# Optimization experiments

Measured on AMD Instinct MI355X. Metric: run time of the kernel, lower is better.

The kernel has to match this reference:

```python
import jax, jax.numpy as jnp
import numpy as np

T, D, I, E, K = 2048, 2048, 5632, 8, 2


def setup_inputs() -> dict:
    key = jax.random.key(0)
    k1, k2, k3, k4, k5 = jax.random.split(key, 5)
    s = 0.02
    return {
        "x": jax.random.normal(k1, (T, D), dtype=jnp.float32),
        "gate_w": jax.random.normal(k2, (E, D), dtype=jnp.float32) * s,
        "w_gate": jax.random.normal(k3, (E, I, D), dtype=jnp.float32) * s,
        "w_up": jax.random.normal(k4, (E, I, D), dtype=jnp.float32) * s,
        "w_down": jax.random.normal(k5, (E, D, I), dtype=jnp.float32) * s,
    }


def reference(x, gate_w, w_gate, w_up, w_down):
    # Router: logits [T, E], top-k then softmax over the k selected logits
    logits = x @ gate_w.T
    top_vals, top_idx = jax.lax.top_k(logits, K)          # [T, K]
    rw = jax.nn.softmax(top_vals, axis=-1)                # [T, K]
    # Dense combine weights [T, E]: sum of routing weights over selected slots.
    # Mathematically identical to the per-(expert, slot) scatter-add in torch,
    # since duplicate selections of the same expert just sum their weights.
    combine = jnp.sum(jax.nn.one_hot(top_idx, E, dtype=x.dtype) * rw[..., None], axis=1)  # [T, E]
    # SwiGLU expert MLPs, batched over experts (grouped GEMM as dense einsum)
    g = jnp.einsum("td,eid->tei", x, w_gate)              # [T, E, I]
    u = jnp.einsum("td,eid->tei", x, w_up)                # [T, E, I]
    h = jax.nn.silu(g) * u                                 # [T, E, I]
    out_e = jnp.einsum("tei,edi->ted", h, w_down)         # [T, E, D]
    return jnp.einsum("ted,te->td", out_e, combine)       # [T, D]
```

## Files before the change

### kernel.cpp

```cpp
#include <hip/hip_runtime.h>
#include <hip/hip_bf16.h>
#include <stdint.h>

#define TTOK 2048
#define DDIM 2048
#define IDIM 5632
#define NEXP 8

typedef __attribute__((ext_vector_type(8))) short bf16x8;
typedef __attribute__((ext_vector_type(4))) float f32x4;
typedef __attribute__((ext_vector_type(8))) unsigned short u16x8;
typedef __attribute__((ext_vector_type(4))) unsigned short u16x4;

__device__ __forceinline__ unsigned short f2bf(float f) {
  union { float f; uint32_t u; } v; v.f = f;
  uint32_t u = v.u + 0x7fffu + ((v.u >> 16) & 1u);
  return (unsigned short)(u >> 16);
}

__device__ __forceinline__ uint32_t fbits(float f) {
  union { float f; uint32_t u; } v; v.f = f; return v.u;
}

__device__ __forceinline__ u16x8 cvt8t(float4 a, float4 b) {
  union { u16x8 v; uint32_t w[4]; } r;
  r.w[0] = __builtin_amdgcn_perm(fbits(a.y), fbits(a.x), 0x07060302);
  r.w[1] = __builtin_amdgcn_perm(fbits(a.w), fbits(a.z), 0x07060302);
  r.w[2] = __builtin_amdgcn_perm(fbits(b.y), fbits(b.x), 0x07060302);
  r.w[3] = __builtin_amdgcn_perm(fbits(b.w), fbits(b.z), 0x07060302);
  return r.v;
}

typedef __attribute__((address_space(3))) void lds_t;
typedef const __attribute__((address_space(1))) void gbl_t;
__device__ __forceinline__ void gload16(const void* g, void* l) {
  __builtin_amdgcn_global_load_lds((gbl_t*)g, (lds_t*)l, 16, 0, 0);
}

#define PIPE_WAIT_BAR() asm volatile("s_waitcnt vmcnt(8) lgkmcnt(0)\n\ts_barrier" ::: "memory")

__global__ __launch_bounds__(256) void router_kernel(
    const float* __restrict__ x, const float* __restrict__ gw,
    unsigned short* __restrict__ xbf,
    int* __restrict__ cnt, int* __restrict__ slots, float* __restrict__ wts)
{
  const int lane = threadIdx.x & 63;
  const int t = (blockIdx.x * blockDim.x + threadIdx.x) >> 6;
  const float* xr = x + (size_t)t * DDIM;
  float acc[NEXP];
#pragma unroll
  for (int e = 0; e < NEXP; ++e) acc[e] = 0.f;
#pragma unroll
  for (int it = 0; it < DDIM / 256; ++it) {
    const int d = (it * 64 + lane) * 4;
    const float4 xv = *(const float4*)(xr + d);
    u16x4 xb; xb[0]=f2bf(xv.x); xb[1]=f2bf(xv.y); xb[2]=f2bf(xv.z); xb[3]=f2bf(xv.w);
    *(u16x4*)(xbf + (size_t)t * DDIM + d) = xb;
#pragma unroll
    for (int e = 0; e < NEXP; ++e) {
      const float4 gv = *(const float4*)(gw + (size_t)e * DDIM + d);
      acc[e] += xv.x*gv.x + xv.y*gv.y + xv.z*gv.z + xv.w*gv.w;
    }
  }
#pragma unroll
  for (int e = 0; e < NEXP; ++e) {
    float v = acc[e];
#pragma unroll
    for (int off = 32; off > 0; off >>= 1) v += __shfl_xor(v, off);
    acc[e] = v;
  }
  if (lane == 0) {
    int i0 = 0; float v0 = acc[0];
#pragma unroll
    for (int e = 1; e < NEXP; ++e) if (acc[e] > v0) { v0 = acc[e]; i0 = e; }
    int i1 = -1; float v1 = -3.4e38f;
#pragma unroll
    for (int e = 0; e < NEXP; ++e) { if (e == i0) continue; if (acc[e] > v1) { v1 = acc[e]; i1 = e; } }
    const float e1 = __expf(v1 - v0);
    const float w0 = 1.f / (1.f + e1);
    const float w1 = e1 / (1.f + e1);
    const int p0 = atomicAdd(&cnt[i0], 1);
    slots[i0 * TTOK + p0] = t * 2;     wts[i0 * TTOK + p0] = w0;
    const int p1 = atomicAdd(&cnt[i1], 1);
    slots[i1 * TTOK + p1] = t * 2 + 1; wts[i1 * TTOK + p1] = w1;
  }
}

__global__ void plan_kernel(const int* __restrict__ cnt,
                            int* __restrict__ tilemap, int* __restrict__ ntiles)
{
  if (threadIdx.x == 0 && blockIdx.x == 0) {
    int n = 0;
#pragma unroll
    for (int e = 0; e < NEXP; ++e) {
      const int nt = (cnt[e] + 255) >> 8;
      for (int m = 0; m < nt; ++m) tilemap[n++] = (e << 8) | m;
    }
    ntiles[0] = n;
  }
}


__global__ __launch_bounds__(512, 2) void gateup_kernel(
    const unsigned short* __restrict__ xbf,
    const float* __restrict__ wg, const float* __restrict__ wu,
    const int* __restrict__ cnt, const int* __restrict__ slots,
    const int* __restrict__ tilemap, const int* __restrict__ ntiles,
    unsigned short* __restrict__ h)
{
  const int flat = (blockIdx.x & 7) * 132 + (blockIdx.x >> 3);
  const int ti = flat % 24;
  if (ti >= ntiles[0]) return;
  const int em = tilemap[ti];
  const int e = em >> 8;
  const int mt = em & 255;
  const int n0 = (flat / 24) * 128;
  const int count = cnt[e];
  const int m0 = mt * 256;

  __shared__ unsigned short A[2][256][64];
  __shared__ unsigned short Bg[2][128][64];
  __shared__ unsigned short Bu[2][128][64];
  __shared__ int rslot[256];
  __shared__ int rtok[256];

  const int tid = threadIdx.x;
  const int lane = tid & 63;
  const int wid = tid >> 6;

  if (tid < 256) {
    const int idx = m0 + tid;
    const int safe = slots[e * TTOK + m0];
    const int s = (idx < count) ? slots[e * TTOK + idx] : safe;
    rslot[tid] = (idx < count) ? s : -1;
    rtok[tid] = s >> 1;
  }
  __syncthreads();

  const int aswz = ((lane & 7) ^ ((lane >> 3) & 7)) * 8;
  const unsigned short* aptr[4];
#pragma unroll
  for (int j = 0; j < 4; ++j) {
    const int arow = j * 64 + wid * 8 + (lane >> 3);
    aptr[j] = xbf + (size_t)rtok[arow] * DDIM + aswz;
  }

  const int brow = tid >> 2;
  const int bcb = (tid & 3) * 2;
  const int bswz = brow & 7;
  const size_t wboff = (size_t)e * IDIM * DDIM + (size_t)(n0 + brow) * DDIM + bcb * 8;
  const float* gsrc = wg + wboff;
  const float* usrc = wu + wboff;

  const int wr = wid >> 2;
  const int wc = wid & 3;
  const int fr = lane & 15;
  const int kc = lane >> 4;
  const int rsw = fr & 7;

  f32x4 accg[8][2] = {};
  f32x4 accu[8][2] = {};

  float4 Pg[4], Pu[4];
#pragma unroll
  for (int j = 0; j < 4; ++j) gload16(aptr[j], &A[0][j * 64 + wid * 8][0]);
#pragma unroll
  for (int q = 0; q < 4; ++q) { Pg[q] = *(const float4*)(gsrc + q * 4); Pu[q] = *(const float4*)(usrc + q * 4); }
#pragma unroll
  for (int qq = 0; qq < 2; ++qq) {
    const int oc = ((bcb + qq) ^ bswz) * 8;
    *(u16x8*)&Bg[0][brow][oc] = cvt8t(Pg[qq * 2], Pg[qq * 2 + 1]);
    *(u16x8*)&Bu[0][brow][oc] = cvt8t(Pu[qq * 2], Pu[qq * 2 + 1]);
  }
#pragma unroll
  for (int q = 0; q < 4; ++q) { Pg[q] = *(const float4*)(gsrc + 64 + q * 4); Pu[q] = *(const float4*)(usrc + 64 + q * 4); }
  PIPE_WAIT_BAR();

#pragma unroll 2
  for (int t = 0; t < 32; ++t) {
    const int cur = t & 1;
    const int kp  = (t + 1 <= 31) ? (t + 1) * 64 : 31 * 64;
    const int kp2 = (t + 2 <= 31) ? (t + 2) * 64 : 31 * 64;

#pragma unroll
    for (int j = 0; j < 4; ++j) gload16(aptr[j] + kp, &A[cur ^ 1][j * 64 + wid * 8][0]);
    __builtin_amdgcn_sched_barrier(0);
#pragma unroll
    for (int qq = 0; qq < 2; ++qq) {
      const int oc = ((bcb + qq) ^ bswz) * 8;
      *(u16x8*)&Bg[cur ^ 1][brow][oc] = cvt8t(Pg[qq * 2], Pg[qq * 2 + 1]);
      *(u16x8*)&Bu[cur ^ 1][brow][oc] = cvt8t(Pu[qq * 2], Pu[qq * 2 + 1]);
    }
#pragma unroll
    for (int q = 0; q < 4; ++q) { Pg[q] = *(const float4*)(gsrc + kp2 + q * 4); Pu[q] = *(const float4*)(usrc + kp2 + q * 4); }
    __builtin_amdgcn_sched_barrier(0);

#pragma unroll
    for (int kk = 0; kk < 2; ++kk) {
      bf16x8 a[8], bg[2], bu[2];
      const int cs = ((kk * 4 + kc) ^ rsw) * 8;
#pragma unroll
      for (int mf = 0; mf < 8; ++mf)
        a[mf] = *(const bf16x8*)&A[cur][wr * 128 + mf * 16 + fr][cs];
#pragma unroll
      for (int nf = 0; nf < 2; ++nf) {
        bg[nf] = *(const bf16x8*)&Bg[cur][wc * 32 + nf * 16 + fr][cs];
        bu[nf] = *(const bf16x8*)&Bu[cur][wc * 32 + nf * 16 + fr][cs];
      }
      __builtin_amdgcn_s_setprio(1);
#pragma unroll
      for (int mf = 0; mf < 8; ++mf)
#pragma unroll
        for (int nf = 0; nf < 2; ++nf) {
          accg[mf][nf] = __builtin_amdgcn_mfma_f32_16x16x32_bf16(a[mf], bg[nf], accg[mf][nf], 0, 0, 0);
          accu[mf][nf] = __builtin_amdgcn_mfma_f32_16x16x32_bf16(a[mf], bu[nf], accu[mf][nf], 0, 0, 0);
        }
      __builtin_amdgcn_s_setprio(0);
    }

    PIPE_WAIT_BAR();
  }

#pragma unroll
  for (int mf = 0; mf < 8; ++mf)
#pragma unroll
    for (int nf = 0; nf < 2; ++nf)
#pragma unroll
      for (int j = 0; j < 4; ++j) {
        const int r = wr * 128 + mf * 16 + (lane >> 4) * 4 + j;
        const int s = rslot[r];
        if (s >= 0) {
          const float g = accg[mf][nf][j];
          const float u = accu[mf][nf][j];
          const float hv = g / (1.f + __expf(-g)) * u;
          h[(size_t)s * IDIM + n0 + wc * 32 + nf * 16 + fr] = f2bf(hv);
        }
      }
}

__global__ __launch_bounds__(512, 2) void down_kernel(
    const unsigned short* __restrict__ h,
    const float* __restrict__ wd,
    const int* __restrict__ cnt, const int* __restrict__ slots,
    const float* __restrict__ wts,
    const int* __restrict__ tilemap, const int* __restrict__ ntiles,
    float* __restrict__ out)
{
  const int flat = (blockIdx.x & 7) * 96 + (blockIdx.x >> 3);
  const int ti = flat % 24;
  if (ti >= ntiles[0]) return;
  const int em = tilemap[ti];
  const int e = em >> 8;
  const int mt = em & 255;
  const int rest = flat / 24;
  const int n0 = (rest & 7) * 256;
  const int kbase = (rest >> 3) * (IDIM / 4);
  const int count = cnt[e];
  const int m0 = mt * 256;

  __shared__ unsigned short A[2][256][64];
  __shared__ unsigned short B[2][256][64];
  __shared__ int rslot[256];
  __shared__ float rw[256];

  const int tid = threadIdx.x;
  const int lane = tid & 63;
  const int wid = tid >> 6;

  if (tid < 256) {
    const int idx = m0 + tid;
    const int safe = slots[e * TTOK + m0];
    const int s = (idx < count) ? slots[e * TTOK + idx] : safe;
    rslot[tid] = (idx < count) ? s : (safe | 0x40000000);
    rw[tid] = (idx < count) ? wts[e * TTOK + idx] : 0.f;
  }
  __syncthreads();

  const int aswz = ((lane & 7) ^ ((lane >> 3) & 7)) * 8;
  const unsigned short* aptr[4];
#pragma unroll
  for (int j = 0; j < 4; ++j) {
    const int arow = j * 64 + wid * 8 + (lane >> 3);
    aptr[j] = h + (size_t)(rslot[arow] & 0x3fffffff) * IDIM + kbase + aswz;
  }

  const int brow = tid >> 1;
  const int bcb = (tid & 1) * 4;
  const int bswz = brow & 7;
  const float* bsrc = wd + (size_t)e * DDIM * IDIM + (size_t)(n0 + brow) * IDIM + kbase + bcb * 8;

  const int wr = wid >> 2;
  const int wc = wid & 3;
  const int fr = lane & 15;
  const int kc = lane >> 4;
  const int rsw = fr & 7;

  f32x4 acc[8][4] = {};

  float4 Pb[8];
#pragma unroll
  for (int j = 0; j < 4; ++j) gload16(aptr[j], &A[0][j * 64 + wid * 8][0]);
#pragma unroll
  for (int q = 0; q < 8; ++q) Pb[q] = *(const float4*)(bsrc + q * 4);
#pragma unroll
  for (int qq = 0; qq < 4; ++qq)
    *(u16x8*)&B[0][brow][((bcb + qq) ^ bswz) * 8] = cvt8t(Pb[qq * 2], Pb[qq * 2 + 1]);
#pragma unroll
  for (int q = 0; q < 8; ++q) Pb[q] = *(const float4*)(bsrc + 64 + q * 4);
  PIPE_WAIT_BAR();

#pragma unroll 2
  for (int t = 0; t < 22; ++t) {
    const int cur = t & 1;
    const int kp  = (t + 1 <= 21) ? (t + 1) * 64 : 21 * 64;
    const int kp2 = (t + 2 <= 21) ? (t + 2) * 64 : 21 * 64;

#pragma unroll
    for (int j = 0; j < 4; ++j) gload16(aptr[j] + kp, &A[cur ^ 1][j * 64 + wid * 8][0]);
    __builtin_amdgcn_sched_barrier(0);
#pragma unroll
    for (int qq = 0; qq < 4; ++qq)
      *(u16x8*)&B[cur ^ 1][brow][((bcb + qq) ^ bswz) * 8] = cvt8t(Pb[qq * 2], Pb[qq * 2 + 1]);
#pragma unroll
    for (int q = 0; q < 8; ++q) Pb[q] = *(const float4*)(bsrc + kp2 + q * 4);
    __builtin_amdgcn_sched_barrier(0);

#pragma unroll
    for (int kk = 0; kk < 2; ++kk) {
      bf16x8 a[8], b[4];
      const int cs = ((kk * 4 + kc) ^ rsw) * 8;
#pragma unroll
      for (int mf = 0; mf < 8; ++mf)
        a[mf] = *(const bf16x8*)&A[cur][wr * 128 + mf * 16 + fr][cs];
#pragma unroll
      for (int nf = 0; nf < 4; ++nf)
        b[nf] = *(const bf16x8*)&B[cur][wc * 64 + nf * 16 + fr][cs];
      __builtin_amdgcn_s_setprio(1);
#pragma unroll
      for (int mf = 0; mf < 8; ++mf)
#pragma unroll
        for (int nf = 0; nf < 4; ++nf)
          acc[mf][nf] = __builtin_amdgcn_mfma_f32_16x16x32_bf16(a[mf], b[nf], acc[mf][nf], 0, 0, 0);
      __builtin_amdgcn_s_setprio(0);
    }

    PIPE_WAIT_BAR();
  }

#pragma unroll
  for (int mf = 0; mf < 8; ++mf)
#pragma unroll
    for (int j = 0; j < 4; ++j) {
      const int r = wr * 128 + mf * 16 + (lane >> 4) * 4 + j;
      const int s = rslot[r];
      if (!(s & 0x40000000)) {
        const int t2 = s >> 1;
        const float w = rw[r];
#pragma unroll
        for (int nf = 0; nf < 4; ++nf)
          atomicAdd(out + (size_t)t2 * DDIM + n0 + wc * 64 + nf * 16 + fr,
                    acc[mf][nf][j] * w);
      }
    }
}

extern "C" void kernel_launch(void* const* d_in, const int* in_sizes, int n_in,
                              void* d_out, int out_size, void* d_ws, size_t ws_size,
                              hipStream_t stream) {
  const float* x  = (const float*)d_in[0];
  const float* gw = (const float*)d_in[1];
  const float* wg = (const float*)d_in[2];
  const float* wu = (const float*)d_in[3];
  const float* wd = (const float*)d_in[4];
  float* out = (float*)d_out;

  char* ws = (char*)d_ws;
  unsigned short* xbf = (unsigned short*)ws;
  unsigned short* h   = (unsigned short*)(ws + 8388608);
  int*   slots = (int*)(ws + 8388608 + 46137344);
  float* wts   = (float*)(ws + 8388608 + 46137344 + 65536);
  int*   cnt   = (int*)(ws + 8388608 + 46137344 + 131072);
  int*   tmap  = (int*)(ws + 8388608 + 46137344 + 131072 + 32);
  int*   ntl   = (int*)(ws + 8388608 + 46137344 + 131072 + 288);

  hipMemsetAsync(cnt, 0, NEXP * sizeof(int), stream);
  hipMemsetAsync(d_out, 0, (size_t)TTOK * DDIM * sizeof(float), stream);

  router_kernel<<<TTOK / 4, 256, 0, stream>>>(x, gw, xbf, cnt, slots, wts);
  plan_kernel<<<1, 64, 0, stream>>>(cnt, tmap, ntl);
  gateup_kernel<<<1056, 512, 0, stream>>>(xbf, wg, wu, cnt, slots, tmap, ntl, h);
  down_kernel<<<768, 512, 0, stream>>>(h, wd, cnt, slots, wts, tmap, ntl, out);
}
```

Before: 816.9 us.

## Restructure MoE GEMM pipelines into phased MFMA/load interleave with contiguous h layout

Both grouped GEMM kernels now split each K step into four barrier-separated phases, each issuing part of the next tile's global loads and LDS writes and then a quarter of the MFMAs. This is meant to overlap memory traffic with matrix work more finely. Gate and up weights share one 256-row B tile with a single accumulator array, and the SiLU*up combine happens through an LDS exchange after the loop. The h intermediate is laid out contiguously per expert using prefix offsets from the plan kernel, so down_kernel reads A rows sequentially instead of gathering by slot. In exchange there are many more barriers per iteration and an extra LDS round trip in the epilogue.

```diff
diff --git a/kernel.cpp b/kernel.cpp
--- a/kernel.cpp
+++ b/kernel.cpp
@@ -37,7 +37,37 @@
   __builtin_amdgcn_global_load_lds((gbl_t*)g, (lds_t*)l, 16, 0, 0);
 }
 
-#define PIPE_WAIT_BAR() asm volatile("s_waitcnt vmcnt(8) lgkmcnt(0)\n\ts_barrier" ::: "memory")
+#define WRITE_B(buf, hh, r0, r1, r2, r3) do {                                  \
+    *(u16x8*)&SB[buf][(hh)*128 + brow][((bcb + 0) ^ bswz) * 8] = cvt8t(r0, r1);\
+    *(u16x8*)&SB[buf][(hh)*128 + brow][((bcb + 1) ^ bswz) * 8] = cvt8t(r2, r3);\
+  } while (0)
+
+#define PHASE(buf, kk, mh, VM8, ...) do {                                      \
+    const int cs_ = (((kk) * 4 + kc) ^ rsw) * 8;                               \
+    bf16x8 afr[4];                                                             \
+    _Pragma("unroll")                                                          \
+    for (int m_ = 0; m_ < 4; ++m_)                                             \
+      afr[m_] = *(const bf16x8*)&SA[buf][wr*128 + ((mh)*4 + m_)*16 + fr][cs_]; \
+    if ((mh) == 0) {                                                           \
+      _Pragma("unroll")                                                        \
+      for (int n_ = 0; n_ < 4; ++n_)                                           \
+        bfr[n_] = *(const bf16x8*)&SB[buf][wc*64 + n_*16 + fr][cs_];           \
+    }                                                                          \
+    __VA_ARGS__;                                                               \
+    if (VM8) { asm volatile("s_waitcnt vmcnt(8)" ::: "memory"); }              \
+    __builtin_amdgcn_s_barrier();                                              \
+    asm volatile("s_waitcnt lgkmcnt(0)" ::: "memory");                         \
+    __builtin_amdgcn_sched_barrier(0);                                         \
+    __builtin_amdgcn_s_setprio(1);                                             \
+    _Pragma("unroll")                                                          \
+    for (int m_ = 0; m_ < 4; ++m_)                                             \
+      _Pragma("unroll")                                                        \
+      for (int n_ = 0; n_ < 4; ++n_)                                           \
+        acc[(mh)*4 + m_][n_] = __builtin_amdgcn_mfma_f32_16x16x32_bf16(        \
+            afr[m_], bfr[n_], acc[(mh)*4 + m_][n_], 0, 0, 0);                  \
+    __builtin_amdgcn_s_setprio(0);                                             \
+    __builtin_amdgcn_s_barrier();                                              \
+  } while (0)
 
 __global__ __launch_bounds__(256) void router_kernel(
     const float* __restrict__ x, const float* __restrict__ gw,
@@ -87,14 +117,17 @@
 }
 
 __global__ void plan_kernel(const int* __restrict__ cnt,
-                            int* __restrict__ tilemap, int* __restrict__ ntiles)
+                            int* __restrict__ tilemap, int* __restrict__ ntiles,
+                            int* __restrict__ po)
 {
   if (threadIdx.x == 0 && blockIdx.x == 0) {
-    int n = 0;
+    int n = 0, off = 0;
 #pragma unroll
     for (int e = 0; e < NEXP; ++e) {
+      po[e] = off;
       const int nt = (cnt[e] + 255) >> 8;
       for (int m = 0; m < nt; ++m) tilemap[n++] = (e << 8) | m;
+      off += nt << 8;
     }
     ntiles[0] = n;
   }
@@ -105,6 +138,7 @@
     const unsigned short* __restrict__ xbf,
     const float* __restrict__ wg, const float* __restrict__ wu,
     const int* __restrict__ cnt, const int* __restrict__ slots,
+    const int* __restrict__ po,
     const int* __restrict__ tilemap, const int* __restrict__ ntiles,
     unsigned short* __restrict__ h)
 {
@@ -117,11 +151,10 @@
   const int n0 = (flat / 24) * 128;
   const int count = cnt[e];
   const int m0 = mt * 256;
-
-  __shared__ unsigned short A[2][256][64];
-  __shared__ unsigned short Bg[2][128][64];
-  __shared__ unsigned short Bu[2][128][64];
-  __shared__ int rslot[256];
+  const int abase = po[e] + m0;
+
+  __shared__ unsigned short SA[2][256][64];
+  __shared__ unsigned short SB[2][256][64];
   __shared__ int rtok[256];
 
   const int tid = threadIdx.x;
@@ -130,27 +163,22 @@
 
   if (tid < 256) {
     const int idx = m0 + tid;
-    const int safe = slots[e * TTOK + m0];
-    const int s = (idx < count) ? slots[e * TTOK + idx] : safe;
-    rslot[tid] = (idx < count) ? s : -1;
-    rtok[tid] = s >> 1;
+    rtok[tid] = (idx < count) ? (slots[e * TTOK + idx] >> 1) : (slots[e * TTOK + m0] >> 1);
   }
   __syncthreads();
 
   const int aswz = ((lane & 7) ^ ((lane >> 3) & 7)) * 8;
-  const unsigned short* aptr[4];
-#pragma unroll
-  for (int j = 0; j < 4; ++j) {
-    const int arow = j * 64 + wid * 8 + (lane >> 3);
-    aptr[j] = xbf + (size_t)rtok[arow] * DDIM + aswz;
-  }
+  const unsigned short* ap00 = xbf + (size_t)rtok[      wid * 16     + (lane >> 3)] * DDIM + aswz;
+  const unsigned short* ap01 = xbf + (size_t)rtok[      wid * 16 + 8 + (lane >> 3)] * DDIM + aswz;
+  const unsigned short* ap10 = xbf + (size_t)rtok[128 + wid * 16     + (lane >> 3)] * DDIM + aswz;
+  const unsigned short* ap11 = xbf + (size_t)rtok[128 + wid * 16 + 8 + (lane >> 3)] * DDIM + aswz;
 
   const int brow = tid >> 2;
   const int bcb = (tid & 3) * 2;
   const int bswz = brow & 7;
-  const size_t wboff = (size_t)e * IDIM * DDIM + (size_t)(n0 + brow) * DDIM + bcb * 8;
-  const float* gsrc = wg + wboff;
-  const float* usrc = wu + wboff;
+  const size_t wo = (size_t)e * IDIM * DDIM + (size_t)(n0 + brow) * DDIM + bcb * 8;
+  const float* gsrc = wg + wo;
+  const float* usrc = wu + wo;
 
   const int wr = wid >> 2;
   const int wc = wid & 3;
@@ -158,91 +186,110 @@
   const int kc = lane >> 4;
   const int rsw = fr & 7;
 
-  f32x4 accg[8][2] = {};
-  f32x4 accu[8][2] = {};
-
-  float4 Pg[4], Pu[4];
-#pragma unroll
-  for (int j = 0; j < 4; ++j) gload16(aptr[j], &A[0][j * 64 + wid * 8][0]);
-#pragma unroll
-  for (int q = 0; q < 4; ++q) { Pg[q] = *(const float4*)(gsrc + q * 4); Pu[q] = *(const float4*)(usrc + q * 4); }
-#pragma unroll
-  for (int qq = 0; qq < 2; ++qq) {
-    const int oc = ((bcb + qq) ^ bswz) * 8;
-    *(u16x8*)&Bg[0][brow][oc] = cvt8t(Pg[qq * 2], Pg[qq * 2 + 1]);
-    *(u16x8*)&Bu[0][brow][oc] = cvt8t(Pu[qq * 2], Pu[qq * 2 + 1]);
-  }
-#pragma unroll
-  for (int q = 0; q < 4; ++q) { Pg[q] = *(const float4*)(gsrc + 64 + q * 4); Pu[q] = *(const float4*)(usrc + 64 + q * 4); }
-  PIPE_WAIT_BAR();
-
-#pragma unroll 2
-  for (int t = 0; t < 32; ++t) {
-    const int cur = t & 1;
-    const int kp  = (t + 1 <= 31) ? (t + 1) * 64 : 31 * 64;
-    const int kp2 = (t + 2 <= 31) ? (t + 2) * 64 : 31 * 64;
-
-#pragma unroll
-    for (int j = 0; j < 4; ++j) gload16(aptr[j] + kp, &A[cur ^ 1][j * 64 + wid * 8][0]);
-    __builtin_amdgcn_sched_barrier(0);
-#pragma unroll
-    for (int qq = 0; qq < 2; ++qq) {
-      const int oc = ((bcb + qq) ^ bswz) * 8;
-      *(u16x8*)&Bg[cur ^ 1][brow][oc] = cvt8t(Pg[qq * 2], Pg[qq * 2 + 1]);
-      *(u16x8*)&Bu[cur ^ 1][brow][oc] = cvt8t(Pu[qq * 2], Pu[qq * 2 + 1]);
-    }
-#pragma unroll
-    for (int q = 0; q < 4; ++q) { Pg[q] = *(const float4*)(gsrc + kp2 + q * 4); Pu[q] = *(const float4*)(usrc + kp2 + q * 4); }
-    __builtin_amdgcn_sched_barrier(0);
-
-#pragma unroll
-    for (int kk = 0; kk < 2; ++kk) {
-      bf16x8 a[8], bg[2], bu[2];
-      const int cs = ((kk * 4 + kc) ^ rsw) * 8;
-#pragma unroll
-      for (int mf = 0; mf < 8; ++mf)
-        a[mf] = *(const bf16x8*)&A[cur][wr * 128 + mf * 16 + fr][cs];
-#pragma unroll
-      for (int nf = 0; nf < 2; ++nf) {
-        bg[nf] = *(const bf16x8*)&Bg[cur][wc * 32 + nf * 16 + fr][cs];
-        bu[nf] = *(const bf16x8*)&Bu[cur][wc * 32 + nf * 16 + fr][cs];
-      }
-      __builtin_amdgcn_s_setprio(1);
-#pragma unroll
-      for (int mf = 0; mf < 8; ++mf)
-#pragma unroll
-        for (int nf = 0; nf < 2; ++nf) {
-          accg[mf][nf] = __builtin_amdgcn_mfma_f32_16x16x32_bf16(a[mf], bg[nf], accg[mf][nf], 0, 0, 0);
-          accu[mf][nf] = __builtin_amdgcn_mfma_f32_16x16x32_bf16(a[mf], bu[nf], accu[mf][nf], 0, 0, 0);
+  f32x4 acc[8][4] = {};
+  bf16x8 bfr[4];
+  float4 Bst[8];
+
+  gload16(ap00, &SA[0][wid * 16][0]);
+  gload16(ap01, &SA[0][wid * 16 + 8][0]);
+  gload16(ap10, &SA[0][128 + wid * 16][0]);
+  gload16(ap11, &SA[0][128 + wid * 16 + 8][0]);
+  Bst[0] = *(const float4*)(gsrc);      Bst[1] = *(const float4*)(gsrc + 4);
+  Bst[2] = *(const float4*)(gsrc + 8);  Bst[3] = *(const float4*)(gsrc + 12);
+  Bst[4] = *(const float4*)(usrc);      Bst[5] = *(const float4*)(usrc + 4);
+  Bst[6] = *(const float4*)(usrc + 8);  Bst[7] = *(const float4*)(usrc + 12);
+  WRITE_B(0, 0, Bst[0], Bst[1], Bst[2], Bst[3]);
+  WRITE_B(0, 1, Bst[4], Bst[5], Bst[6], Bst[7]);
+  Bst[0] = *(const float4*)(gsrc + 64);      Bst[1] = *(const float4*)(gsrc + 68);
+  Bst[2] = *(const float4*)(gsrc + 72);      Bst[3] = *(const float4*)(gsrc + 76);
+  Bst[4] = *(const float4*)(usrc + 64);      Bst[5] = *(const float4*)(usrc + 68);
+  Bst[6] = *(const float4*)(usrc + 72);      Bst[7] = *(const float4*)(usrc + 76);
+  asm volatile("s_waitcnt lgkmcnt(0)" ::: "memory");
+  __builtin_amdgcn_s_barrier();
+
+#pragma unroll 1
+  for (int it = 0; it < 16; ++it) {
+    const int t = 2 * it;
+    const int k1 = (t + 1) * 64;
+    const int k2 = ((t + 2 < 32) ? t + 2 : 31) * 64;
+    const int k3 = ((t + 3 < 32) ? t + 3 : 31) * 64;
+
+    PHASE(0, 0, 0, 0,
+      gload16(ap00 + k1, &SA[1][wid * 16][0]);
+      gload16(ap01 + k1, &SA[1][wid * 16 + 8][0]);
+      WRITE_B(1, 0, Bst[0], Bst[1], Bst[2], Bst[3]));
+    PHASE(0, 0, 1, 0,
+      gload16(ap10 + k1, &SA[1][128 + wid * 16][0]);
+      gload16(ap11 + k1, &SA[1][128 + wid * 16 + 8][0]);
+      WRITE_B(1, 1, Bst[4], Bst[5], Bst[6], Bst[7]));
+    PHASE(0, 1, 0, 0,
+      Bst[0] = *(const float4*)(gsrc + k2);
+      Bst[1] = *(const float4*)(gsrc + k2 + 4);
+      Bst[2] = *(const float4*)(gsrc + k2 + 8);
+      Bst[3] = *(const float4*)(gsrc + k2 + 12));
+    PHASE(0, 1, 1, 1,
+      Bst[4] = *(const float4*)(usrc + k2);
+      Bst[5] = *(const float4*)(usrc + k2 + 4);
+      Bst[6] = *(const float4*)(usrc + k2 + 8);
+      Bst[7] = *(const float4*)(usrc + k2 + 12));
+    PHASE(1, 0, 0, 0,
+      gload16(ap00 + k2, &SA[0][wid * 16][0]);
+      gload16(ap01 + k2, &SA[0][wid * 16 + 8][0]);
+      WRITE_B(0, 0, Bst[0], Bst[1], Bst[2], Bst[3]));
+    PHASE(1, 0, 1, 0,
+      gload16(ap10 + k2, &SA[0][128 + wid * 16][0]);
+      gload16(ap11 + k2, &SA[0][128 + wid * 16 + 8][0]);
+      WRITE_B(0, 1, Bst[4], Bst[5], Bst[6], Bst[7]));
+    PHASE(1, 1, 0, 0,
+      Bst[0] = *(const float4*)(gsrc + k3);
+      Bst[1] = *(const float4*)(gsrc + k3 + 4);
+      Bst[2] = *(const float4*)(gsrc + k3 + 8);
+      Bst[3] = *(const float4*)(gsrc + k3 + 12));
+    PHASE(1, 1, 1, 1,
+      Bst[4] = *(const float4*)(usrc + k3);
+      Bst[5] = *(const float4*)(usrc + k3 + 4);
+      Bst[6] = *(const float4*)(usrc + k3 + 8);
+      Bst[7] = *(const float4*)(usrc + k3 + 12));
+  }
+
+  __syncthreads();
+  if (wc >= 2) {
+    float* uex = (wc == 2) ? (float*)&SA[0][0][0] : (float*)&SB[0][0][0];
+#pragma unroll
+    for (int mf = 0; mf < 8; ++mf)
+#pragma unroll
+      for (int nf = 0; nf < 4; ++nf)
+#pragma unroll
+        for (int j = 0; j < 4; ++j) {
+          const int r = wr * 128 + mf * 16 + (lane >> 4) * 4 + j;
+          uex[r * 64 + nf * 16 + fr] = acc[mf][nf][j];
         }
-      __builtin_amdgcn_s_setprio(0);
-    }
-
-    PIPE_WAIT_BAR();
-  }
-
-#pragma unroll
-  for (int mf = 0; mf < 8; ++mf)
-#pragma unroll
-    for (int nf = 0; nf < 2; ++nf)
-#pragma unroll
-      for (int j = 0; j < 4; ++j) {
-        const int r = wr * 128 + mf * 16 + (lane >> 4) * 4 + j;
-        const int s = rslot[r];
-        if (s >= 0) {
-          const float g = accg[mf][nf][j];
-          const float u = accu[mf][nf][j];
-          const float hv = g / (1.f + __expf(-g)) * u;
-          h[(size_t)s * IDIM + n0 + wc * 32 + nf * 16 + fr] = f2bf(hv);
+  }
+  __syncthreads();
+  if (wc < 2) {
+    const float* uex = (wc == 0) ? (const float*)&SA[0][0][0] : (const float*)&SB[0][0][0];
+#pragma unroll
+    for (int mf = 0; mf < 8; ++mf)
+#pragma unroll
+      for (int nf = 0; nf < 4; ++nf)
+#pragma unroll
+        for (int j = 0; j < 4; ++j) {
+          const int r = wr * 128 + mf * 16 + (lane >> 4) * 4 + j;
+          if (m0 + r < count) {
+            const float g = acc[mf][nf][j];
+            const float u = uex[r * 64 + nf * 16 + fr];
+            const float hv = g / (1.f + __expf(-g)) * u;
+            h[(size_t)(abase + r) * IDIM + n0 + wc * 64 + nf * 16 + fr] = f2bf(hv);
+          }
         }
-      }
+  }
 }
 
 __global__ __launch_bounds__(512, 2) void down_kernel(
-    const unsigned short* __restrict__ h,
+    const unsigned short* __restrict__ hb,
     const float* __restrict__ wd,
     const int* __restrict__ cnt, const int* __restrict__ slots,
-    const float* __restrict__ wts,
+    const float* __restrict__ wts, const int* __restrict__ po,
     const int* __restrict__ tilemap, const int* __restrict__ ntiles,
     float* __restrict__ out)
 {
@@ -254,13 +301,14 @@
   const int mt = em & 255;
   const int rest = flat / 24;
   const int n0 = (rest & 7) * 256;
-  const int kbase = (rest >> 3) * (IDIM / 4);
+  const int kbase = (rest >> 3) * 1408;
   const int count = cnt[e];
   const int m0 = mt * 256;
-
-  __shared__ unsigned short A[2][256][64];
-  __shared__ unsigned short B[2][256][64];
-  __shared__ int rslot[256];
+  const int abase = po[e] + m0;
+
+  __shared__ unsigned short SA[2][256][64];
+  __shared__ unsigned short SB[2][256][64];
+  __shared__ int rtok[256];
   __shared__ float rw[256];
 
   const int tid = threadIdx.x;
@@ -269,25 +317,21 @@
 
   if (tid < 256) {
     const int idx = m0 + tid;
-    const int safe = slots[e * TTOK + m0];
-    const int s = (idx < count) ? slots[e * TTOK + idx] : safe;
-    rslot[tid] = (idx < count) ? s : (safe | 0x40000000);
+    rtok[tid] = (idx < count) ? (slots[e * TTOK + idx] >> 1) : 0;
     rw[tid] = (idx < count) ? wts[e * TTOK + idx] : 0.f;
   }
-  __syncthreads();
 
   const int aswz = ((lane & 7) ^ ((lane >> 3) & 7)) * 8;
-  const unsigned short* aptr[4];
-#pragma unroll
-  for (int j = 0; j < 4; ++j) {
-    const int arow = j * 64 + wid * 8 + (lane >> 3);
-    aptr[j] = h + (size_t)(rslot[arow] & 0x3fffffff) * IDIM + kbase + aswz;
-  }
-
-  const int brow = tid >> 1;
-  const int bcb = (tid & 1) * 4;
+  const unsigned short* ap00 = hb + (size_t)(abase +       wid * 16     + (lane >> 3)) * IDIM + kbase + aswz;
+  const unsigned short* ap01 = hb + (size_t)(abase +       wid * 16 + 8 + (lane >> 3)) * IDIM + kbase + aswz;
+  const unsigned short* ap10 = hb + (size_t)(abase + 128 + wid * 16     + (lane >> 3)) * IDIM + kbase + aswz;
+  const unsigned short* ap11 = hb + (size_t)(abase + 128 + wid * 16 + 8 + (lane >> 3)) * IDIM + kbase + aswz;
+
+  const int brow = tid >> 2;
+  const int bcb = (tid & 3) * 2;
   const int bswz = brow & 7;
-  const float* bsrc = wd + (size_t)e * DDIM * IDIM + (size_t)(n0 + brow) * IDIM + kbase + bcb * 8;
+  const float* bsrc0 = wd + (size_t)e * DDIM * IDIM + (size_t)(n0 + brow) * IDIM + kbase + bcb * 8;
+  const float* bsrc1 = wd + (size_t)e * DDIM * IDIM + (size_t)(n0 + 128 + brow) * IDIM + kbase + bcb * 8;
 
   const int wr = wid >> 2;
   const int wc = wid & 3;
@@ -296,55 +340,69 @@
   const int rsw = fr & 7;
 
   f32x4 acc[8][4] = {};
-
-  float4 Pb[8];
-#pragma unroll
-  for (int j = 0; j < 4; ++j) gload16(aptr[j], &A[0][j * 64 + wid * 8][0]);
-#pragma unroll
-  for (int q = 0; q < 8; ++q) Pb[q] = *(const float4*)(bsrc + q * 4);
-#pragma unroll
-  for (int qq = 0; qq < 4; ++qq)
-    *(u16x8*)&B[0][brow][((bcb + qq) ^ bswz) * 8] = cvt8t(Pb[qq * 2], Pb[qq * 2 + 1]);
-#pragma unroll
-  for (int q = 0; q < 8; ++q) Pb[q] = *(const float4*)(bsrc + 64 + q * 4);
-  PIPE_WAIT_BAR();
-
-#pragma unroll 2
-  for (int t = 0; t < 22; ++t) {
-    const int cur = t & 1;
-    const int kp  = (t + 1 <= 21) ? (t + 1) * 64 : 21 * 64;
-    const int kp2 = (t + 2 <= 21) ? (t + 2) * 64 : 21 * 64;
-
-#pragma unroll
-    for (int j = 0; j < 4; ++j) gload16(aptr[j] + kp, &A[cur ^ 1][j * 64 + wid * 8][0]);
-    __builtin_amdgcn_sched_barrier(0);
-#pragma unroll
-    for (int qq = 0; qq < 4; ++qq)
-      *(u16x8*)&B[cur ^ 1][brow][((bcb + qq) ^ bswz) * 8] = cvt8t(Pb[qq * 2], Pb[qq * 2 + 1]);
-#pragma unroll
-    for (int q = 0; q < 8; ++q) Pb[q] = *(const float4*)(bsrc + kp2 + q * 4);
-    __builtin_amdgcn_sched_barrier(0);
-
-#pragma unroll
-    for (int kk = 0; kk < 2; ++kk) {
-      bf16x8 a[8], b[4];
-      const int cs = ((kk * 4 + kc) ^ rsw) * 8;
-#pragma unroll
-      for (int mf = 0; mf < 8; ++mf)
-        a[mf] = *(const bf16x8*)&A[cur][wr * 128 + mf * 16 + fr][cs];
-#pragma unroll
-      for (int nf = 0; nf < 4; ++nf)
-        b[nf] = *(const bf16x8*)&B[cur][wc * 64 + nf * 16 + fr][cs];
-      __builtin_amdgcn_s_setprio(1);
-#pragma unroll
-      for (int mf = 0; mf < 8; ++mf)
-#pragma unroll
-        for (int nf = 0; nf < 4; ++nf)
-          acc[mf][nf] = __builtin_amdgcn_mfma_f32_16x16x32_bf16(a[mf], b[nf], acc[mf][nf], 0, 0, 0);
-      __builtin_amdgcn_s_setprio(0);
-    }
-
-    PIPE_WAIT_BAR();
+  bf16x8 bfr[4];
+  float4 Bst[8];
+
+  gload16(ap00, &SA[0][wid * 16][0]);
+  gload16(ap01, &SA[0][wid * 16 + 8][0]);
+  gload16(ap10, &SA[0][128 + wid * 16][0]);
+  gload16(ap11, &SA[0][128 + wid * 16 + 8][0]);
+  Bst[0] = *(const float4*)(bsrc0);      Bst[1] = *(const float4*)(bsrc0 + 4);
+  Bst[2] = *(const float4*)(bsrc0 + 8);  Bst[3] = *(const float4*)(bsrc0 + 12);
+  Bst[4] = *(const float4*)(bsrc1);      Bst[5] = *(const float4*)(bsrc1 + 4);
+  Bst[6] = *(const float4*)(bsrc1 + 8);  Bst[7] = *(const float4*)(bsrc1 + 12);
+  WRITE_B(0, 0, Bst[0], Bst[1], Bst[2], Bst[3]);
+  WRITE_B(0, 1, Bst[4], Bst[5], Bst[6], Bst[7]);
+  Bst[0] = *(const float4*)(bsrc0 + 64);      Bst[1] = *(const float4*)(bsrc0 + 68);
+  Bst[2] = *(const float4*)(bsrc0 + 72);      Bst[3] = *(const float4*)(bsrc0 + 76);
+  Bst[4] = *(const float4*)(bsrc1 + 64);      Bst[5] = *(const float4*)(bsrc1 + 68);
+  Bst[6] = *(const float4*)(bsrc1 + 72);      Bst[7] = *(const float4*)(bsrc1 + 76);
+  asm volatile("s_waitcnt lgkmcnt(0)" ::: "memory");
+  __builtin_amdgcn_s_barrier();
+
+#pragma unroll 1
+  for (int it = 0; it < 11; ++it) {
+    const int t = 2 * it;
+    const int k1 = (t + 1) * 64;
+    const int k2 = ((t + 2 < 22) ? t + 2 : 21) * 64;
+    const int k3 = ((t + 3 < 22) ? t + 3 : 21) * 64;
+
+    PHASE(0, 0, 0, 0,
+      gload16(ap00 + k1, &SA[1][wid * 16][0]);
+      gload16(ap01 + k1, &SA[1][wid * 16 + 8][0]);
+      WRITE_B(1, 0, Bst[0], Bst[1], Bst[2], Bst[3]));
+    PHASE(0, 0, 1, 0,
+      gload16(ap10 + k1, &SA[1][128 + wid * 16][0]);
+      gload16(ap11 + k1, &SA[1][128 + wid * 16 + 8][0]);
+      WRITE_B(1, 1, Bst[4], Bst[5], Bst[6], Bst[7]));
+    PHASE(0, 1, 0, 0,
+      Bst[0] = *(const float4*)(bsrc0 + k2);
+      Bst[1] = *(const float4*)(bsrc0 + k2 + 4);
+      Bst[2] = *(const float4*)(bsrc0 + k2 + 8);
+      Bst[3] = *(const float4*)(bsrc0 + k2 + 12));
+    PHASE(0, 1, 1, 1,
+      Bst[4] = *(const float4*)(bsrc1 + k2);
+      Bst[5] = *(const float4*)(bsrc1 + k2 + 4);
+      Bst[6] = *(const float4*)(bsrc1 + k2 + 8);
+      Bst[7] = *(const float4*)(bsrc1 + k2 + 12));
+    PHASE(1, 0, 0, 0,
+      gload16(ap00 + k2, &SA[0][wid * 16][0]);
+      gload16(ap01 + k2, &SA[0][wid * 16 + 8][0]);
+      WRITE_B(0, 0, Bst[0], Bst[1], Bst[2], Bst[3]));
+    PHASE(1, 0, 1, 0,
+      gload16(ap10 + k2, &SA[0][128 + wid * 16][0]);
+      gload16(ap11 + k2, &SA[0][128 + wid * 16 + 8][0]);
+      WRITE_B(0, 1, Bst[4], Bst[5], Bst[6], Bst[7]));
+    PHASE(1, 1, 0, 0,
+      Bst[0] = *(const float4*)(bsrc0 + k3);
+      Bst[1] = *(const float4*)(bsrc0 + k3 + 4);
+      Bst[2] = *(const float4*)(bsrc0 + k3 + 8);
+      Bst[3] = *(const float4*)(bsrc0 + k3 + 12));
+    PHASE(1, 1, 1, 1,
+      Bst[4] = *(const float4*)(bsrc1 + k3);
+      Bst[5] = *(const float4*)(bsrc1 + k3 + 4);
+      Bst[6] = *(const float4*)(bsrc1 + k3 + 8);
+      Bst[7] = *(const float4*)(bsrc1 + k3 + 12));
   }
 
 #pragma unroll
@@ -352,9 +410,8 @@
 #pragma unroll
     for (int j = 0; j < 4; ++j) {
       const int r = wr * 128 + mf * 16 + (lane >> 4) * 4 + j;
-      const int s = rslot[r];
-      if (!(s & 0x40000000)) {
-        const int t2 = s >> 1;
+      if (m0 + r < count) {
+        const int t2 = rtok[r];
         const float w = rw[r];
 #pragma unroll
         for (int nf = 0; nf < 4; ++nf)
@@ -377,17 +434,18 @@
   char* ws = (char*)d_ws;
   unsigned short* xbf = (unsigned short*)ws;
   unsigned short* h   = (unsigned short*)(ws + 8388608);
-  int*   slots = (int*)(ws + 8388608 + 46137344);
-  float* wts   = (float*)(ws + 8388608 + 46137344 + 65536);
-  int*   cnt   = (int*)(ws + 8388608 + 46137344 + 131072);
-  int*   tmap  = (int*)(ws + 8388608 + 46137344 + 131072 + 32);
-  int*   ntl   = (int*)(ws + 8388608 + 46137344 + 131072 + 288);
+  int*   slots = (int*)(ws + 77594624);
+  float* wts   = (float*)(ws + 77660160);
+  int*   cnt   = (int*)(ws + 77725696);
+  int*   tmap  = (int*)(ws + 77725728);
+  int*   ntl   = (int*)(ws + 77725856);
+  int*   po    = (int*)(ws + 77725860);
 
   hipMemsetAsync(cnt, 0, NEXP * sizeof(int), stream);
   hipMemsetAsync(d_out, 0, (size_t)TTOK * DDIM * sizeof(float), stream);
 
   router_kernel<<<TTOK / 4, 256, 0, stream>>>(x, gw, xbf, cnt, slots, wts);
-  plan_kernel<<<1, 64, 0, stream>>>(cnt, tmap, ntl);
-  gateup_kernel<<<1056, 512, 0, stream>>>(xbf, wg, wu, cnt, slots, tmap, ntl, h);
-  down_kernel<<<768, 512, 0, stream>>>(h, wd, cnt, slots, wts, tmap, ntl, out);
-}
+  plan_kernel<<<1, 64, 0, stream>>>(cnt, tmap, ntl, po);
+  gateup_kernel<<<1056, 512, 0, stream>>>(xbf, wg, wu, cnt, slots, po, tmap, ntl, h);
+  down_kernel<<<768, 512, 0, stream>>>(h, wd, cnt, slots, wts, po, tmap, ntl, out);
+}
```

Result: slower. 889.2 us (+8.9%).
